# Kernel optimization log

Measured on AMD Instinct MI355X. Metric: run time of the kernel, lower is better.

The kernel has to match this reference:

```python
import jax, jax.numpy as jnp
import numpy as np


def _proj(x, w, b):
    # 1x1 conv as channel matmul: x (n,c,h,w), w (k,c), b (k,) -> (n,k,h,w)
    return jnp.einsum('nchw,kc->nkhw', x, w) + b[None, :, None, None]


def setup_inputs() -> dict:
    key = jax.random.key(0)
    ks = jax.random.split(key, 9)
    cin, cinter = 256, 128
    n, h, w = 4, 64, 64
    s = lambda fan_in: 1.0 / np.sqrt(fan_in)
    return {
        'x': jax.random.normal(ks[0], (n, cin, h, w), jnp.float32),
        'theta_w': jax.random.normal(ks[1], (cinter, cin), jnp.float32) * s(cin),
        'theta_b': jax.random.normal(ks[2], (cinter,), jnp.float32) * 0.01,
        'phi_w': jax.random.normal(ks[3], (cinter, cin), jnp.float32) * s(cin),
        'phi_b': jax.random.normal(ks[4], (cinter,), jnp.float32) * 0.01,
        'g_w': jax.random.normal(ks[5], (cinter, cin), jnp.float32) * s(cin),
        'g_b': jax.random.normal(ks[6], (cinter,), jnp.float32) * 0.01,
        'w_w': jax.random.normal(ks[7], (cin, cinter), jnp.float32) * s(cinter),
        'w_b': jax.random.normal(ks[8], (cin,), jnp.float32) * 0.01,
    }


def reference(x, theta_w, theta_b, phi_w, phi_b, g_w, g_b, w_w, w_b):
    n, c, h, w = x.shape
    cinter = theta_w.shape[0]
    hw = h * w
    theta_x = _proj(x, theta_w, theta_b).reshape(n, cinter, hw)  # (n,ci,HW)
    phi_x = _proj(x, phi_w, phi_b).reshape(n, cinter, hw)        # (n,ci,HW)
    g_x = _proj(x, g_w, g_b).reshape(n, cinter, hw)              # (n,ci,HW)
    # f_x = phi^T @ theta : (n, HW, HW), softmax over last dim (theta positions)
    f_x = jnp.einsum('nci,ncj->nij', phi_x, theta_x)
    f_x = jax.nn.softmax(f_x, axis=-1)
    # attended = g @ f : (n, ci, HW)
    att = jnp.einsum('nci,nij->ncj', g_x, f_x).reshape(n, cinter, h, w)
    res_x = _proj(att, w_w, w_b)  # (n, c, h, w)
    return x + res_x
```

## Files before the change

kernel.cpp:

```cpp
#include <hip/hip_runtime.h>
#include <hip/hip_bf16.h>

#define B_ 4
#define C_ 256
#define CI_ 128
#define P_ 4096
#define LOG2E 1.44269504088896340736f

typedef __attribute__((ext_vector_type(8))) _Float16 half8;
typedef __attribute__((ext_vector_type(2))) __fp16 fp16x2;
typedef __attribute__((ext_vector_type(8))) short short8;
typedef __attribute__((ext_vector_type(4))) short short4v;
typedef __attribute__((ext_vector_type(4))) float floatx4;

__device__ __forceinline__ float bf2f(ushort h) {
  union { unsigned u; float f; } v; v.u = ((unsigned)h) << 16; return v.f;
}
__device__ __forceinline__ ushort f2bf(float f) {
  union { float f; unsigned u; } v; v.f = f;
  unsigned r = v.u + 0x7FFFu + ((v.u >> 16) & 1u);
  return (ushort)(r >> 16);
}
__device__ __forceinline__ ushort f2h(float f) {
  _Float16 h = (_Float16)f;
  union { _Float16 h; ushort u; } v; v.h = h; return v.u;
}
__device__ __forceinline__ uint2 pk4h(float a, float b, float c, float d) {
  union { fp16x2 h[2]; uint2 u; } pk;
  pk.h[0] = __builtin_amdgcn_cvt_pkrtz(a, b);
  pk.h[1] = __builtin_amdgcn_cvt_pkrtz(c, d);
  return pk.u;
}

#define MFMA16(a, b, c) __builtin_amdgcn_mfma_f32_16x16x32_f16((a), (b), (c), 0, 0, 0)

__device__ __forceinline__ int detect_bf16(const ushort* __restrict__ xu) {
  __shared__ int cnt_;
  if (threadIdx.x == 0) cnt_ = 0;
  __syncthreads();
  int local = 0;
  int t = threadIdx.x & 255;
#pragma unroll
  for (int s = 0; s < 8; ++s) {
    ushort u = xu[(t * 8 + s) * 2];
    int e = (u >> 7) & 0xFF;
    local += (e >= 0x70 && e <= 0x84) ? 1 : 0;
  }
  atomicAdd(&cnt_, local);
  __syncthreads();
  return cnt_ > 1024;
}

__global__ void k_trc(const void* __restrict__ xv, ushort* __restrict__ xT,
                      const void* __restrict__ s0, const void* __restrict__ s1,
                      const void* __restrict__ s2, const void* __restrict__ s3,
                      const void* __restrict__ tbv, const void* __restrict__ pbv,
                      const void* __restrict__ gbv, const void* __restrict__ wbv,
                      ushort* __restrict__ dstW, float* __restrict__ biasf) {
  int is_bf16 = detect_bf16((const ushort*)xv);
  int bid = blockIdx.x;
  int t = threadIdx.x;
  if (bid < 1024) {
    __shared__ __align__(16) ushort tile[64][72];
    int pb = (bid & 63) * 64;
    int cb = ((bid >> 6) & 3) * 64;
    int b = bid >> 8;
#pragma unroll
    for (int it = 0; it < 2; ++it) {
      int lin = it * 256 + t;
      int c = lin >> 3;
      int p = (lin & 7) * 8;
      size_t base = ((size_t)(b * C_) + cb + c) * P_ + pb + p;
      float vv[8];
      if (is_bf16) {
        short8 v = *(const short8*)((const ushort*)xv + base);
#pragma unroll
        for (int i = 0; i < 8; ++i) vv[i] = bf2f((ushort)v[i]);
      } else {
        const float* xf = (const float*)xv;
        float4 v0 = *(const float4*)(xf + base);
        float4 v1 = *(const float4*)(xf + base + 4);
        vv[0] = v0.x; vv[1] = v0.y; vv[2] = v0.z; vv[3] = v0.w;
        vv[4] = v1.x; vv[5] = v1.y; vv[6] = v1.z; vv[7] = v1.w;
      }
#pragma unroll
      for (int i = 0; i < 8; ++i) {
        int iw = (i + t) & 7;
        tile[p + iw][c] = f2h(vv[iw]);
      }
    }
    __syncthreads();
#pragma unroll
    for (int it = 0; it < 2; ++it) {
      int lin = it * 256 + t;
      int p = lin >> 3;
      int c = (lin & 7) * 8;
      short8 v = *(const short8*)&tile[p][c];
      *(short8*)(xT + ((size_t)(b * P_) + pb + p) * C_ + cb + c) = v;
    }
  } else if (bid < 1536) {
    int wid = bid - 1024;
    int a = wid >> 7;
    const void* srcs[4] = {s0, s1, s2, s3};
    int i = (wid & 127) * 256 + t;
    float v = is_bf16 ? bf2f(((const ushort*)srcs[a])[i]) : ((const float*)srcs[a])[i];
    dstW[a * 32768 + i] = f2h(v);
  } else {
    int idx = (bid - 1536) * 256 + t;
    if (idx < 640) {
      const void* src; int loc;
      if (idx < 128)      { src = tbv; loc = idx; }
      else if (idx < 256) { src = pbv; loc = idx - 128; }
      else if (idx < 384) { src = gbv; loc = idx - 256; }
      else                { src = wbv; loc = idx - 384; }
      float v = is_bf16 ? bf2f(((const ushort*)src)[loc]) : ((const float*)src)[loc];
      biasf[idx] = v;
    }
  }
}

__global__ __launch_bounds__(256, 4) void k_proj(
    const ushort* __restrict__ xT, const ushort* __restrict__ Wh,
    const float* __restrict__ biasf,
    ushort* __restrict__ thetaT, ushort* __restrict__ phiT,
    ushort* __restrict__ g) {
  int t = threadIdx.x;
  int w = t >> 6, lane = t & 63, l = lane & 15, q = lane >> 4;
  int pblk = blockIdx.x * 32;
  int b = blockIdx.y;
  floatx4 acc[2][6];
#pragma unroll
  for (int ps = 0; ps < 2; ++ps)
#pragma unroll
    for (int ks = 0; ks < 6; ++ks) acc[ps][ks] = (floatx4){0.f, 0.f, 0.f, 0.f};
  const ushort* xrow[2];
#pragma unroll
  for (int ps = 0; ps < 2; ++ps)
    xrow[ps] = xT + ((size_t)(b * P_) + pblk + ps * 16 + l) * C_;
  const ushort* wrow[6];
  int prj[6], kloc[6];
#pragma unroll
  for (int ks = 0; ks < 6; ++ks) {
    int kg = w * 96 + ks * 16;
    prj[ks] = kg >> 7;
    kloc[ks] = kg & 127;
    wrow[ks] = Wh + prj[ks] * 32768 + (size_t)(kloc[ks] + l) * C_;
  }
  for (int c = 0; c < C_; c += 32) {
    half8 av[2], wv[6];
#pragma unroll
    for (int ps = 0; ps < 2; ++ps) av[ps] = *(const half8*)(xrow[ps] + c + q * 8);
#pragma unroll
    for (int ks = 0; ks < 6; ++ks) wv[ks] = *(const half8*)(wrow[ks] + c + q * 8);
#pragma unroll
    for (int ps = 0; ps < 2; ++ps)
#pragma unroll
      for (int ks = 0; ks < 6; ++ks)
        acc[ps][ks] = MFMA16(av[ps], wv[ks], acc[ps][ks]);
  }
#pragma unroll
  for (int ks = 0; ks < 6; ++ks) {
    float bias = biasf[prj[ks] * 128 + kloc[ks] + l];
#pragma unroll
    for (int ps = 0; ps < 2; ++ps) {
      floatx4 d = acc[ps][ks];
      if (prj[ks] < 2) {
        ushort* dst = (prj[ks] == 0 ? thetaT : phiT) +
                      ((size_t)(b * P_) + pblk + ps * 16 + q * 4) * CI_ + kloc[ks] + l;
#pragma unroll
        for (int r = 0; r < 4; ++r) dst[(size_t)r * CI_] = f2h(d[r] + bias);
      } else {
        ushort* dst = g + ((size_t)(b * CI_) + kloc[ks] + l) * P_ + pblk + ps * 16 + q * 4;
        short4v pk;
#pragma unroll
        for (int r = 0; r < 4; ++r) pk[r] = (short)f2h(d[r] + bias);
        *(short4v*)dst = pk;
      }
    }
  }
}

__global__ __launch_bounds__(256, 2) void k_stats(
    const ushort* __restrict__ phiT, const ushort* __restrict__ thetaT,
    float* __restrict__ part) {
  int t = threadIdx.x, w = t >> 6, lane = t & 63, l = lane & 15, q = lane >> 4;
  int i0 = blockIdx.x * 256, j0 = blockIdx.y * 512, b = blockIdx.z;
  half8 av[4][4];
#pragma unroll
  for (int is = 0; is < 4; ++is) {
    const ushort* pr = phiT + ((size_t)(b * P_) + i0 + w * 64 + is * 16 + l) * CI_;
#pragma unroll
    for (int ks = 0; ks < 4; ++ks) av[is][ks] = *(const half8*)(pr + ks * 32 + q * 8);
  }
  float sum[4][4];
#pragma unroll
  for (int is = 0; is < 4; ++is)
#pragma unroll
    for (int r = 0; r < 4; ++r) sum[is][r] = 0.f;
  const ushort* tb0 = thetaT + (size_t)b * P_ * CI_;
  for (int jc = 0; jc < 16; ++jc) {
    int j = j0 + jc * 32;
    half8 bv[2][4];
#pragma unroll
    for (int js = 0; js < 2; ++js) {
      const ushort* tr = tb0 + (size_t)(j + js * 16 + l) * CI_;
#pragma unroll
      for (int ks = 0; ks < 4; ++ks) bv[js][ks] = *(const half8*)(tr + ks * 32 + q * 8);
    }
    floatx4 accS[4][2];
#pragma unroll
    for (int is = 0; is < 4; ++is)
#pragma unroll
      for (int js = 0; js < 2; ++js) accS[is][js] = (floatx4){0.f, 0.f, 0.f, 0.f};
#pragma unroll
    for (int ks = 0; ks < 4; ++ks)
#pragma unroll
      for (int is = 0; is < 4; ++is)
#pragma unroll
        for (int js = 0; js < 2; ++js)
          accS[is][js] = MFMA16(av[is][ks], bv[js][ks], accS[is][js]);
#pragma unroll
    for (int is = 0; is < 4; ++is)
#pragma unroll
      for (int js = 0; js < 2; ++js)
#pragma unroll
        for (int r = 0; r < 4; ++r)
          sum[is][r] += exp2f(fmaf(accS[is][js][r], LOG2E, -64.f));
  }
#pragma unroll
  for (int d = 1; d < 16; d <<= 1)
#pragma unroll
    for (int is = 0; is < 4; ++is)
#pragma unroll
      for (int r = 0; r < 4; ++r) sum[is][r] += __shfl_xor(sum[is][r], d, 64);
  if (l == 0) {
#pragma unroll
    for (int is = 0; is < 4; ++is)
#pragma unroll
      for (int r = 0; r < 4; ++r)
        part[((size_t)blockIdx.y * B_ + b) * P_ + i0 + w * 64 + is * 16 + q * 4 + r] =
            sum[is][r];
  }
}

__global__ void k_lse(const float* __restrict__ part, float* __restrict__ o2) {
  int idx = blockIdx.x * 256 + threadIdx.x;
  float s = 0.f;
#pragma unroll
  for (int p = 0; p < 8; ++p) s += part[(size_t)p * (B_ * P_) + idx];
  o2[idx] = log2f(s) + 64.f;
}

__global__ __launch_bounds__(256, 2) void k_attn(
    const ushort* __restrict__ phiT, const ushort* __restrict__ thetaT,
    const ushort* __restrict__ g, const float* __restrict__ o2,
    ushort* __restrict__ attPA, ushort* __restrict__ attPB, int nChunk) {
  __shared__ __align__(16) ushort thL[128][136];
  __shared__ __align__(16) ushort eL[128][136];
  int t = threadIdx.x;
  int w = t >> 6, lane = t & 63, l = lane & 15, q = lane >> 4;
  int j0 = blockIdx.x * 128, ih = blockIdx.y, b = blockIdx.z;
#pragma unroll
  for (int it = 0; it < 8; ++it) {
    int lin = it * 256 + t, row = lin >> 4, cg = (lin & 15) * 8;
    *(short8*)&thL[row][cg] =
        *(const short8*)(thetaT + ((size_t)(b * P_) + j0 + row) * CI_ + cg);
  }
  floatx4 accA[2][8];
#pragma unroll
  for (int cs = 0; cs < 2; ++cs)
#pragma unroll
    for (int js = 0; js < 8; ++js) accA[cs][js] = (floatx4){0.f, 0.f, 0.f, 0.f};
  __syncthreads();
  const float* orow = o2 + b * P_;
  int istart = ih * nChunk * 128;
  half8 af[2][4];
  float ov[2][4];
#pragma unroll
  for (int is = 0; is < 2; ++is) {
    int iG = istart + w * 32 + is * 16;
    const ushort* pr = phiT + ((size_t)(b * P_) + iG + l) * CI_;
#pragma unroll
    for (int ks = 0; ks < 4; ++ks) af[is][ks] = *(const half8*)(pr + ks * 32 + q * 8);
#pragma unroll
    for (int r = 0; r < 4; ++r) ov[is][r] = orow[iG + q * 4 + r];
  }
  for (int ic = 0; ic < nChunk; ++ic) {
    int ibase = istart + ic * 128;
    half8 gf[2][4];
#pragma unroll
    for (int cs = 0; cs < 2; ++cs) {
      const ushort* gr = g + ((size_t)(b * CI_) + w * 32 + cs * 16 + l) * P_ + ibase;
#pragma unroll
      for (int ks = 0; ks < 4; ++ks) gf[cs][ks] = *(const half8*)(gr + ks * 32 + q * 8);
    }
    floatx4 accS[2][8];
#pragma unroll
    for (int is = 0; is < 2; ++is)
#pragma unroll
      for (int js = 0; js < 8; ++js) accS[is][js] = (floatx4){0.f, 0.f, 0.f, 0.f};
#pragma unroll
    for (int ks = 0; ks < 4; ++ks) {
      half8 bf[8];
#pragma unroll
      for (int js = 0; js < 8; ++js) bf[js] = *(const half8*)&thL[js * 16 + l][ks * 32 + q * 8];
#pragma unroll
      for (int is = 0; is < 2; ++is)
#pragma unroll
        for (int js = 0; js < 8; ++js) accS[is][js] = MFMA16(af[is][ks], bf[js], accS[is][js]);
    }
    uint2 ep[2][8];
#pragma unroll
    for (int is = 0; is < 2; ++is)
#pragma unroll
      for (int js = 0; js < 8; ++js) {
        float e0 = exp2f(fmaf(accS[is][js][0], LOG2E, -ov[is][0]));
        float e1 = exp2f(fmaf(accS[is][js][1], LOG2E, -ov[is][1]));
        float e2 = exp2f(fmaf(accS[is][js][2], LOG2E, -ov[is][2]));
        float e3 = exp2f(fmaf(accS[is][js][3], LOG2E, -ov[is][3]));
        ep[is][js] = pk4h(e0, e1, e2, e3);
      }
    __syncthreads();
#pragma unroll
    for (int is = 0; is < 2; ++is)
#pragma unroll
      for (int js = 0; js < 8; ++js)
        *(uint2*)&eL[js * 16 + l][w * 32 + is * 16 + q * 4] = ep[is][js];
    __syncthreads();
    if (ic < nChunk - 1) {
      int nb = istart + (ic + 1) * 128;
#pragma unroll
      for (int is = 0; is < 2; ++is) {
        int iG = nb + w * 32 + is * 16;
        const ushort* pr = phiT + ((size_t)(b * P_) + iG + l) * CI_;
#pragma unroll
        for (int ks = 0; ks < 4; ++ks) af[is][ks] = *(const half8*)(pr + ks * 32 + q * 8);
#pragma unroll
        for (int r = 0; r < 4; ++r) ov[is][r] = orow[iG + q * 4 + r];
      }
    }
#pragma unroll
    for (int ks = 0; ks < 4; ++ks) {
      half8 ef[8];
#pragma unroll
      for (int js = 0; js < 8; ++js) ef[js] = *(const half8*)&eL[js * 16 + l][ks * 32 + q * 8];
#pragma unroll
      for (int cs = 0; cs < 2; ++cs)
#pragma unroll
        for (int js = 0; js < 8; ++js) accA[cs][js] = MFMA16(gf[cs][ks], ef[js], accA[cs][js]);
    }
  }
  ushort* ap = (ih < 2 ? attPA : attPB) + (size_t)(ih & 1) * (B_ * P_ * CI_);
#pragma unroll
  for (int cs = 0; cs < 2; ++cs)
#pragma unroll
    for (int js = 0; js < 8; ++js) {
      uint2 pk = pk4h(accA[cs][js][0], accA[cs][js][1], accA[cs][js][2], accA[cs][js][3]);
      *(uint2*)(ap + ((size_t)(b * P_) + j0 + js * 16 + l) * CI_ +
                w * 32 + cs * 16 + q * 4) = pk;
    }
}

__global__ __launch_bounds__(256, 4) void k_out(
    const ushort* __restrict__ attPA, const ushort* __restrict__ attPB, int nIH,
    const ushort* __restrict__ wwh, const float* __restrict__ biasf,
    const void* __restrict__ xv, void* __restrict__ outv) {
  int is_bf16 = detect_bf16((const ushort*)xv);
  int t = threadIdx.x;
  int w = t >> 6, lane = t & 63, l = lane & 15, q = lane >> 4;
  int p0 = blockIdx.x * 32, b = blockIdx.y;
  floatx4 accR[4][2];
#pragma unroll
  for (int kk = 0; kk < 4; ++kk)
#pragma unroll
    for (int js = 0; js < 2; ++js) accR[kk][js] = (floatx4){0.f, 0.f, 0.f, 0.f};
#pragma unroll
  for (int ks = 0; ks < 4; ++ks) {
    half8 wf[4], af[2];
#pragma unroll
    for (int kk = 0; kk < 4; ++kk)
      wf[kk] = *(const half8*)(wwh + (size_t)(w * 64 + kk * 16 + l) * CI_ + ks * 32 + q * 8);
#pragma unroll
    for (int js = 0; js < 2; ++js) {
      size_t off = ((size_t)(b * P_) + p0 + js * 16 + l) * CI_ + ks * 32 + q * 8;
      half8 s = *(const half8*)(attPA + off);
      s = s + *(const half8*)(attPA + (size_t)(B_ * P_) * CI_ + off);
      if (nIH == 4) {
        s = s + *(const half8*)(attPB + off);
        s = s + *(const half8*)(attPB + (size_t)(B_ * P_) * CI_ + off);
      }
      af[js] = s;
    }
#pragma unroll
    for (int kk = 0; kk < 4; ++kk)
#pragma unroll
      for (int js = 0; js < 2; ++js) accR[kk][js] = MFMA16(wf[kk], af[js], accR[kk][js]);
  }
#pragma unroll
  for (int kk = 0; kk < 4; ++kk)
#pragma unroll
    for (int r = 0; r < 4; ++r) {
      int c = w * 64 + kk * 16 + q * 4 + r;
      float bias = biasf[384 + c];
#pragma unroll
      for (int js = 0; js < 2; ++js) {
        int p = p0 + js * 16 + l;
        size_t idx = ((size_t)(b * C_) + c) * P_ + p;
        float val = accR[kk][js][r] + bias;
        if (is_bf16) {
          ((ushort*)outv)[idx] = f2bf(bf2f(((const ushort*)xv)[idx]) + val);
        } else {
          ((float*)outv)[idx] = ((const float*)xv)[idx] + val;
        }
      }
    }
}

extern "C" void kernel_launch(void* const* d_in, const int* in_sizes, int n_in,
                              void* d_out, int out_size, void* d_ws, size_t ws_size,
                              hipStream_t stream) {
  const void* x  = d_in[0];
  const void* tw = d_in[1];
  const void* tb = d_in[2];
  const void* pw = d_in[3];
  const void* pb = d_in[4];
  const void* gw = d_in[5];
  const void* gb = d_in[6];
  const void* ww = d_in[7];
  const void* wb = d_in[8];
  char* ws = (char*)d_ws;
  float*  o2     = (float*)(ws);
  float*  part   = (float*)(ws + (64u << 10));
  ushort* Wh     = (ushort*)(ws + (576u << 10));
  float*  biasf  = (float*)(ws + (832u << 10));
  ushort* xT     = (ushort*)(ws + (1u << 20));
  ushort* attPA  = xT;
  ushort* thetaT = (ushort*)(ws + (9u << 20));
  ushort* phiT   = (ushort*)(ws + (13u << 20));
  ushort* gbuf   = (ushort*)(ws + (17u << 20));
  ushort* attPB  = (ushort*)(ws + (21u << 20));
  int big = (ws_size >= (30u << 20)) ? 1 : 0;

  k_trc<<<1539, 256, 0, stream>>>(x, xT, tw, pw, gw, ww, tb, pb, gb, wb, Wh, biasf);
  k_proj<<<dim3(128, 4), 256, 0, stream>>>(xT, Wh, biasf, thetaT, phiT, gbuf);
  k_stats<<<dim3(16, 8, 4), 256, 0, stream>>>(phiT, thetaT, part);
  k_lse<<<64, 256, 0, stream>>>(part, o2);
  if (big) {
    k_attn<<<dim3(32, 4, 4), 256, 0, stream>>>(phiT, thetaT, gbuf, o2, attPA, attPB, 8);
    k_out<<<dim3(128, 4), 256, 0, stream>>>(attPA, attPB, 4, Wh + 3 * 32768, biasf, x, d_out);
  } else {
    k_attn<<<dim3(32, 2, 4), 256, 0, stream>>>(phiT, thetaT, gbuf, o2, attPA, attPB, 16);
    k_out<<<dim3(128, 4), 256, 0, stream>>>(attPA, attPB, 2, Wh + 3 * 32768, biasf, x, d_out);
  }
}
```

Baseline: 232.9 us.

## Restructure attention kernel to per-wave j-tiles with register bpermute instead of LDS

The attention kernel is rewritten so each wave owns 32 theta columns held in registers and walks i in 32-row chunks. The exponentiated scores are redistributed into MFMA B-operand layout with ds_bpermute, which removes the shared-memory staging buffers and both block-wide barriers per chunk. In exchange, every wave now loads its own phi, g and o2 fragments from global memory (four times the redundant traffic across waves), and the chunk count rises to match. The transpose tile padding in k_trc is also changed from 72 to 74 to alter bank mapping.

```diff
diff --git a/kernel.cpp b/kernel.cpp
--- a/kernel.cpp
+++ b/kernel.cpp
@@ -61,7 +61,7 @@
   int bid = blockIdx.x;
   int t = threadIdx.x;
   if (bid < 1024) {
-    __shared__ __align__(16) ushort tile[64][72];
+    __shared__ __align__(16) ushort tile[64][74];
     int pb = (bid & 63) * 64;
     int cb = ((bid >> 6) & 3) * 64;
     int b = bid >> 8;
@@ -255,109 +255,95 @@
     const ushort* __restrict__ phiT, const ushort* __restrict__ thetaT,
     const ushort* __restrict__ g, const float* __restrict__ o2,
     ushort* __restrict__ attPA, ushort* __restrict__ attPB, int nChunk) {
-  __shared__ __align__(16) ushort thL[128][136];
-  __shared__ __align__(16) ushort eL[128][136];
   int t = threadIdx.x;
   int w = t >> 6, lane = t & 63, l = lane & 15, q = lane >> 4;
   int j0 = blockIdx.x * 128, ih = blockIdx.y, b = blockIdx.z;
-#pragma unroll
-  for (int it = 0; it < 8; ++it) {
-    int lin = it * 256 + t, row = lin >> 4, cg = (lin & 15) * 8;
-    *(short8*)&thL[row][cg] =
-        *(const short8*)(thetaT + ((size_t)(b * P_) + j0 + row) * CI_ + cg);
-  }
-  floatx4 accA[2][8];
-#pragma unroll
-  for (int cs = 0; cs < 2; ++cs)
-#pragma unroll
-    for (int js = 0; js < 8; ++js) accA[cs][js] = (floatx4){0.f, 0.f, 0.f, 0.f};
-  __syncthreads();
+  int jw0 = j0 + w * 32;
+  half8 tf[2][4];
+#pragma unroll
+  for (int js = 0; js < 2; ++js) {
+    const ushort* tr = thetaT + ((size_t)(b * P_) + jw0 + js * 16 + l) * CI_;
+#pragma unroll
+    for (int ks = 0; ks < 4; ++ks) tf[js][ks] = *(const half8*)(tr + ks * 32 + q * 8);
+  }
+  floatx4 accA[8][2];
+#pragma unroll
+  for (int cs = 0; cs < 8; ++cs)
+#pragma unroll
+    for (int js = 0; js < 2; ++js) accA[cs][js] = (floatx4){0.f, 0.f, 0.f, 0.f};
   const float* orow = o2 + b * P_;
-  int istart = ih * nChunk * 128;
-  half8 af[2][4];
-  float ov[2][4];
-#pragma unroll
-  for (int is = 0; is < 2; ++is) {
-    int iG = istart + w * 32 + is * 16;
-    const ushort* pr = phiT + ((size_t)(b * P_) + iG + l) * CI_;
-#pragma unroll
-    for (int ks = 0; ks < 4; ++ks) af[is][ks] = *(const half8*)(pr + ks * 32 + q * 8);
-#pragma unroll
-    for (int r = 0; r < 4; ++r) ov[is][r] = orow[iG + q * 4 + r];
-  }
+  int istart = ih * nChunk * 32;
+  int addrA = ((lane >> 4) & 1) * 128 + l * 4;
+  int addrB = addrA + 64;
+  int hiSel = (lane >= 32);
   for (int ic = 0; ic < nChunk; ++ic) {
-    int ibase = istart + ic * 128;
-    half8 gf[2][4];
-#pragma unroll
-    for (int cs = 0; cs < 2; ++cs) {
-      const ushort* gr = g + ((size_t)(b * CI_) + w * 32 + cs * 16 + l) * P_ + ibase;
-#pragma unroll
-      for (int ks = 0; ks < 4; ++ks) gf[cs][ks] = *(const half8*)(gr + ks * 32 + q * 8);
-    }
-    floatx4 accS[2][8];
+    int ibase = istart + ic * 32;
+    half8 af[2][4];
+#pragma unroll
+    for (int is = 0; is < 2; ++is) {
+      const ushort* pr = phiT + ((size_t)(b * P_) + ibase + is * 16 + l) * CI_;
+#pragma unroll
+      for (int ks = 0; ks < 4; ++ks) af[is][ks] = *(const half8*)(pr + ks * 32 + q * 8);
+    }
+    half8 gf[8];
+#pragma unroll
+    for (int cs = 0; cs < 8; ++cs)
+      gf[cs] = *(const half8*)(g + ((size_t)(b * CI_) + cs * 16 + l) * P_ + ibase + q * 8);
+    float4 ov[2];
 #pragma unroll
     for (int is = 0; is < 2; ++is)
-#pragma unroll
-      for (int js = 0; js < 8; ++js) accS[is][js] = (floatx4){0.f, 0.f, 0.f, 0.f};
-#pragma unroll
-    for (int ks = 0; ks < 4; ++ks) {
-      half8 bf[8];
-#pragma unroll
-      for (int js = 0; js < 8; ++js) bf[js] = *(const half8*)&thL[js * 16 + l][ks * 32 + q * 8];
+      ov[is] = *(const float4*)(orow + ibase + is * 16 + q * 4);
+    floatx4 accS[2][2];
+#pragma unroll
+    for (int is = 0; is < 2; ++is)
+#pragma unroll
+      for (int js = 0; js < 2; ++js) accS[is][js] = (floatx4){0.f, 0.f, 0.f, 0.f};
+#pragma unroll
+    for (int ks = 0; ks < 4; ++ks)
 #pragma unroll
       for (int is = 0; is < 2; ++is)
 #pragma unroll
-        for (int js = 0; js < 8; ++js) accS[is][js] = MFMA16(af[is][ks], bf[js], accS[is][js]);
-    }
-    uint2 ep[2][8];
+        for (int js = 0; js < 2; ++js)
+          accS[is][js] = MFMA16(af[is][ks], tf[js][ks], accS[is][js]);
+    uint pkv[2][2][2];
 #pragma unroll
     for (int is = 0; is < 2; ++is)
 #pragma unroll
-      for (int js = 0; js < 8; ++js) {
-        float e0 = exp2f(fmaf(accS[is][js][0], LOG2E, -ov[is][0]));
-        float e1 = exp2f(fmaf(accS[is][js][1], LOG2E, -ov[is][1]));
-        float e2 = exp2f(fmaf(accS[is][js][2], LOG2E, -ov[is][2]));
-        float e3 = exp2f(fmaf(accS[is][js][3], LOG2E, -ov[is][3]));
-        ep[is][js] = pk4h(e0, e1, e2, e3);
-      }
-    __syncthreads();
-#pragma unroll
-    for (int is = 0; is < 2; ++is)
-#pragma unroll
-      for (int js = 0; js < 8; ++js)
-        *(uint2*)&eL[js * 16 + l][w * 32 + is * 16 + q * 4] = ep[is][js];
-    __syncthreads();
-    if (ic < nChunk - 1) {
-      int nb = istart + (ic + 1) * 128;
-#pragma unroll
-      for (int is = 0; is < 2; ++is) {
-        int iG = nb + w * 32 + is * 16;
-        const ushort* pr = phiT + ((size_t)(b * P_) + iG + l) * CI_;
-#pragma unroll
-        for (int ks = 0; ks < 4; ++ks) af[is][ks] = *(const half8*)(pr + ks * 32 + q * 8);
-#pragma unroll
-        for (int r = 0; r < 4; ++r) ov[is][r] = orow[iG + q * 4 + r];
-      }
-    }
-#pragma unroll
-    for (int ks = 0; ks < 4; ++ks) {
-      half8 ef[8];
-#pragma unroll
-      for (int js = 0; js < 8; ++js) ef[js] = *(const half8*)&eL[js * 16 + l][ks * 32 + q * 8];
-#pragma unroll
-      for (int cs = 0; cs < 2; ++cs)
-#pragma unroll
-        for (int js = 0; js < 8; ++js) accA[cs][js] = MFMA16(gf[cs][ks], ef[js], accA[cs][js]);
+      for (int js = 0; js < 2; ++js) {
+        float e0 = exp2f(fmaf(accS[is][js][0], LOG2E, -ov[is].x));
+        float e1 = exp2f(fmaf(accS[is][js][1], LOG2E, -ov[is].y));
+        float e2 = exp2f(fmaf(accS[is][js][2], LOG2E, -ov[is].z));
+        float e3 = exp2f(fmaf(accS[is][js][3], LOG2E, -ov[is].w));
+        uint2 u = pk4h(e0, e1, e2, e3);
+        pkv[is][js][0] = u.x;
+        pkv[is][js][1] = u.y;
+      }
+#pragma unroll
+    for (int js = 0; js < 2; ++js) {
+      int w0a = __builtin_amdgcn_ds_bpermute(addrA, (int)pkv[0][js][0]);
+      int w0b = __builtin_amdgcn_ds_bpermute(addrA, (int)pkv[1][js][0]);
+      int w1a = __builtin_amdgcn_ds_bpermute(addrA, (int)pkv[0][js][1]);
+      int w1b = __builtin_amdgcn_ds_bpermute(addrA, (int)pkv[1][js][1]);
+      int w2a = __builtin_amdgcn_ds_bpermute(addrB, (int)pkv[0][js][0]);
+      int w2b = __builtin_amdgcn_ds_bpermute(addrB, (int)pkv[1][js][0]);
+      int w3a = __builtin_amdgcn_ds_bpermute(addrB, (int)pkv[0][js][1]);
+      int w3b = __builtin_amdgcn_ds_bpermute(addrB, (int)pkv[1][js][1]);
+      union { uint4 u; half8 h; } ef;
+      ef.u.x = (uint)(hiSel ? w0b : w0a);
+      ef.u.y = (uint)(hiSel ? w1b : w1a);
+      ef.u.z = (uint)(hiSel ? w2b : w2a);
+      ef.u.w = (uint)(hiSel ? w3b : w3a);
+#pragma unroll
+      for (int cs = 0; cs < 8; ++cs) accA[cs][js] = MFMA16(gf[cs], ef.h, accA[cs][js]);
     }
   }
   ushort* ap = (ih < 2 ? attPA : attPB) + (size_t)(ih & 1) * (B_ * P_ * CI_);
 #pragma unroll
-  for (int cs = 0; cs < 2; ++cs)
-#pragma unroll
-    for (int js = 0; js < 8; ++js) {
+  for (int cs = 0; cs < 8; ++cs)
+#pragma unroll
+    for (int js = 0; js < 2; ++js) {
       uint2 pk = pk4h(accA[cs][js][0], accA[cs][js][1], accA[cs][js][2], accA[cs][js][3]);
-      *(uint2*)(ap + ((size_t)(b * P_) + j0 + js * 16 + l) * CI_ +
-                w * 32 + cs * 16 + q * 4) = pk;
+      *(uint2*)(ap + ((size_t)(b * P_) + jw0 + js * 16 + l) * CI_ + cs * 16 + q * 4) = pk;
     }
 }
 
@@ -446,10 +432,10 @@
   k_stats<<<dim3(16, 8, 4), 256, 0, stream>>>(phiT, thetaT, part);
   k_lse<<<64, 256, 0, stream>>>(part, o2);
   if (big) {
-    k_attn<<<dim3(32, 4, 4), 256, 0, stream>>>(phiT, thetaT, gbuf, o2, attPA, attPB, 8);
+    k_attn<<<dim3(32, 4, 4), 256, 0, stream>>>(phiT, thetaT, gbuf, o2, attPA, attPB, 32);
     k_out<<<dim3(128, 4), 256, 0, stream>>>(attPA, attPB, 4, Wh + 3 * 32768, biasf, x, d_out);
   } else {
-    k_attn<<<dim3(32, 2, 4), 256, 0, stream>>>(phiT, thetaT, gbuf, o2, attPA, attPB, 16);
+    k_attn<<<dim3(32, 2, 4), 256, 0, stream>>>(phiT, thetaT, gbuf, o2, attPA, attPB, 64);
     k_out<<<dim3(128, 4), 256, 0, stream>>>(attPA, attPB, 2, Wh + 3 * 32768, biasf, x, d_out);
   }
 }
```

After: 298.8 us. +28.3%, slower.

## Remap stats/attn workgroups to XCDs for L2 locality, add MFMA priority hints

Applied to the files above, without the earlier changes.

Flattens the k_stats and k_attn grids to 1D and remaps workgroup IDs so that blocks sharing the same batch and key/query slice are placed on the same XCD, which is meant to improve per-XCD L2 reuse of phiT, thetaT and g. It also raises wave priority around the MFMA loops in k_attn with s_setprio so matrix work issues ahead of the exp and LDS phases. The transpose tile in k_trc is padded to 74 columns to change its LDS bank mapping. The remapping assumes workgroups are dispatched round-robin across 8 XCDs, and it relies on nIH being 2 or 4.

```diff
diff --git a/kernel.cpp b/kernel.cpp
--- a/kernel.cpp
+++ b/kernel.cpp
@@ -61,7 +61,7 @@
   int bid = blockIdx.x;
   int t = threadIdx.x;
   if (bid < 1024) {
-    __shared__ __align__(16) ushort tile[64][72];
+    __shared__ __align__(16) ushort tile[64][74];
     int pb = (bid & 63) * 64;
     int cb = ((bid >> 6) & 3) * 64;
     int b = bid >> 8;
@@ -184,7 +184,13 @@
     const ushort* __restrict__ phiT, const ushort* __restrict__ thetaT,
     float* __restrict__ part) {
   int t = threadIdx.x, w = t >> 6, lane = t & 63, l = lane & 15, q = lane >> 4;
-  int i0 = blockIdx.x * 256, j0 = blockIdx.y * 512, b = blockIdx.z;
+  int wgid = blockIdx.x;
+  int xcd = wgid & 7, slot = wgid >> 3;
+  int st = xcd + 8 * (slot >> 4);
+  int i0 = (slot & 15) * 256;
+  int jsp = st & 7;
+  int j0 = jsp * 512;
+  int b = st >> 3;
   half8 av[4][4];
 #pragma unroll
   for (int is = 0; is < 4; ++is) {
@@ -238,7 +244,7 @@
     for (int is = 0; is < 4; ++is)
 #pragma unroll
       for (int r = 0; r < 4; ++r)
-        part[((size_t)blockIdx.y * B_ + b) * P_ + i0 + w * 64 + is * 16 + q * 4 + r] =
+        part[((size_t)jsp * B_ + b) * P_ + i0 + w * 64 + is * 16 + q * 4 + r] =
             sum[is][r];
   }
 }
@@ -254,12 +260,18 @@
 __global__ __launch_bounds__(256, 2) void k_attn(
     const ushort* __restrict__ phiT, const ushort* __restrict__ thetaT,
     const ushort* __restrict__ g, const float* __restrict__ o2,
-    ushort* __restrict__ attPA, ushort* __restrict__ attPB, int nChunk) {
+    ushort* __restrict__ attPA, ushort* __restrict__ attPB,
+    int nIH, int nChunk) {
   __shared__ __align__(16) ushort thL[128][136];
   __shared__ __align__(16) ushort eL[128][136];
   int t = threadIdx.x;
   int w = t >> 6, lane = t & 63, l = lane & 15, q = lane >> 4;
-  int j0 = blockIdx.x * 128, ih = blockIdx.y, b = blockIdx.z;
+  int wgid = blockIdx.x;
+  int xcd = wgid & 7, slot = wgid >> 3;
+  int st = xcd + 8 * (slot >> 5);
+  int j0 = (slot & 31) * 128;
+  int ih = st & (nIH - 1);
+  int b = st >> ((nIH == 4) ? 2 : 1);
 #pragma unroll
   for (int it = 0; it < 8; ++it) {
     int lin = it * 256 + t, row = lin >> 4, cg = (lin & 15) * 8;
@@ -299,6 +311,7 @@
     for (int is = 0; is < 2; ++is)
 #pragma unroll
       for (int js = 0; js < 8; ++js) accS[is][js] = (floatx4){0.f, 0.f, 0.f, 0.f};
+    __builtin_amdgcn_s_setprio(1);
 #pragma unroll
     for (int ks = 0; ks < 4; ++ks) {
       half8 bf[8];
@@ -309,6 +322,7 @@
 #pragma unroll
         for (int js = 0; js < 8; ++js) accS[is][js] = MFMA16(af[is][ks], bf[js], accS[is][js]);
     }
+    __builtin_amdgcn_s_setprio(0);
     uint2 ep[2][8];
 #pragma unroll
     for (int is = 0; is < 2; ++is)
@@ -339,6 +353,7 @@
         for (int r = 0; r < 4; ++r) ov[is][r] = orow[iG + q * 4 + r];
       }
     }
+    __builtin_amdgcn_s_setprio(1);
 #pragma unroll
     for (int ks = 0; ks < 4; ++ks) {
       half8 ef[8];
@@ -349,6 +364,7 @@
 #pragma unroll
         for (int js = 0; js < 8; ++js) accA[cs][js] = MFMA16(gf[cs][ks], ef[js], accA[cs][js]);
     }
+    __builtin_amdgcn_s_setprio(0);
   }
   ushort* ap = (ih < 2 ? attPA : attPB) + (size_t)(ih & 1) * (B_ * P_ * CI_);
 #pragma unroll
@@ -443,13 +459,13 @@
 
   k_trc<<<1539, 256, 0, stream>>>(x, xT, tw, pw, gw, ww, tb, pb, gb, wb, Wh, biasf);
   k_proj<<<dim3(128, 4), 256, 0, stream>>>(xT, Wh, biasf, thetaT, phiT, gbuf);
-  k_stats<<<dim3(16, 8, 4), 256, 0, stream>>>(phiT, thetaT, part);
+  k_stats<<<512, 256, 0, stream>>>(phiT, thetaT, part);
   k_lse<<<64, 256, 0, stream>>>(part, o2);
   if (big) {
-    k_attn<<<dim3(32, 4, 4), 256, 0, stream>>>(phiT, thetaT, gbuf, o2, attPA, attPB, 8);
+    k_attn<<<512, 256, 0, stream>>>(phiT, thetaT, gbuf, o2, attPA, attPB, 4, 8);
     k_out<<<dim3(128, 4), 256, 0, stream>>>(attPA, attPB, 4, Wh + 3 * 32768, biasf, x, d_out);
   } else {
-    k_attn<<<dim3(32, 2, 4), 256, 0, stream>>>(phiT, thetaT, gbuf, o2, attPA, attPB, 16);
+    k_attn<<<256, 256, 0, stream>>>(phiT, thetaT, gbuf, o2, attPA, attPB, 2, 16);
     k_out<<<dim3(128, 4), 256, 0, stream>>>(attPA, attPB, 2, Wh + 3 * 32768, biasf, x, d_out);
   }
 }
```

Measured after the change: 227.4 us. 2.3% less time.
